# Kernel optimization log

Measured on AMD Instinct MI355X. Metric: run time of the kernel, lower is better.

## Reference

```python
import jax, jax.numpy as jnp
import numpy as np

EPS = 1e-5

def _conv(x, w, b, pad):
    y = jax.lax.conv_general_dilated(x, w, window_strides=(1, 1),
                                     padding=[(pad, pad), (pad, pad)],
                                     dimension_numbers=('NCHW', 'OIHW', 'NCHW'))
    return y + b[None, :, None, None]

def _bn_train(x, gamma, beta):
    # BatchNorm2d in training mode: batch statistics over (N,H,W), biased var
    mean = jnp.mean(x, axis=(0, 2, 3), keepdims=True)
    var = jnp.mean(jnp.square(x - mean), axis=(0, 2, 3), keepdims=True)
    xhat = (x - mean) * jax.lax.rsqrt(var + EPS)
    return xhat * gamma[None, :, None, None] + beta[None, :, None, None]

def _maxpool2(x):
    # CustomMaxPool2d(kernel=2) -> stride=2, no padding applied to data
    return jax.lax.reduce_window(x, -jnp.inf, jax.lax.max,
                                 (1, 1, 2, 2), (1, 1, 2, 2), 'VALID')

def setup_inputs() -> dict:
    key = jax.random.key(0)
    ks = jax.random.split(key, 12)
    B = 64
    d = jax.random.normal(ks[0], (B, 3, 224, 224), dtype=jnp.float32)
    def w_init(k, shape, fan_in):
        bound = 1.0 / np.sqrt(fan_in)
        return jax.random.uniform(k, shape, jnp.float32, -bound, bound)
    conv1_w = w_init(ks[1], (16, 3, 2, 2), 3 * 2 * 2)
    conv1_b = w_init(ks[2], (16,), 3 * 2 * 2)
    conv2_w = w_init(ks[3], (32, 16, 3, 3), 16 * 9)
    conv2_b = w_init(ks[4], (32,), 16 * 9)
    conv3_w = w_init(ks[5], (64, 32, 3, 3), 32 * 9)
    conv3_b = w_init(ks[6], (64,), 32 * 9)
    fc1_w = w_init(ks[7], (256, 64 * 28 * 28), 64 * 28 * 28)
    fc1_b = w_init(ks[8], (256,), 64 * 28 * 28)
    fc2_w = w_init(ks[9], (5, 256), 256)
    fc2_b = w_init(ks[10], (5,), 256)
    return dict(d=d,
                conv1_w=conv1_w, conv1_b=conv1_b,
                bn1_g=jnp.ones((16,), jnp.float32), bn1_b=jnp.zeros((16,), jnp.float32),
                conv2_w=conv2_w, conv2_b=conv2_b,
                bn2_g=jnp.ones((32,), jnp.float32), bn2_b=jnp.zeros((32,), jnp.float32),
                conv3_w=conv3_w, conv3_b=conv3_b,
                bn3_g=jnp.ones((64,), jnp.float32), bn3_b=jnp.zeros((64,), jnp.float32),
                fc1_w=fc1_w, fc1_b=fc1_b, fc2_w=fc2_w, fc2_b=fc2_b)

def reference(d, conv1_w, conv1_b, bn1_g, bn1_b,
              conv2_w, conv2_b, bn2_g, bn2_b,
              conv3_w, conv3_b, bn3_g, bn3_b,
              fc1_w, fc1_b, fc2_w, fc2_b):
    x = _maxpool2(jax.nn.relu(_bn_train(_conv(d, conv1_w, conv1_b, 1), bn1_g, bn1_b)))   # [B,16,112,112]
    x = _maxpool2(jax.nn.relu(_bn_train(_conv(x, conv2_w, conv2_b, 1), bn2_g, bn2_b)))   # [B,32,56,56]
    x = _maxpool2(jax.nn.relu(_bn_train(_conv(x, conv3_w, conv3_b, 1), bn3_g, bn3_b)))   # [B,64,28,28]
    x = x.reshape(x.shape[0], -1)                                                        # [B,50176]
    x = jax.nn.relu(x @ fc1_w.T + fc1_b)
    return x @ fc2_w.T + fc2_b                                                           # [B,5]
```

## Files before the change

### kernel.cpp

```cpp
#include <hip/hip_runtime.h>
#include <cstdint>
#include <cstddef>


typedef __attribute__((ext_vector_type(8))) short sh8_t;
typedef __attribute__((ext_vector_type(4))) float f4_t;
typedef unsigned short u16;
typedef unsigned int u32;

#define WS_X1   ((size_t)0)
#define WS_SEL1 ((size_t)6422528)
#define WS_X2   ((size_t)12845056)
#define WS_SEL2 ((size_t)16056320)
#define WS_X3T  ((size_t)19267584)
#define WS_SEL3 ((size_t)20873216)
#define WS_WT1  ((size_t)22478848)
#define WS_WT2  ((size_t)22479360)
#define WS_WT3  ((size_t)22482432)
#define WS_P1   ((size_t)22491648)
#define WS_P2   ((size_t)24334848)
#define WS_P3   ((size_t)25137664)
#define WS_PD   ((size_t)25596416)
#define WS_ST   ((size_t)25600512)
#define WS_FCP  ((size_t)25600736)
#define WS_H1   ((size_t)26518240)

static __device__ __forceinline__ float4 ldg4(const float* p) {
  return *reinterpret_cast<const float4*>(p);
}
static __device__ __forceinline__ float bf2f(u16 u) {
  union { u32 i; float f; } c; c.i = ((u32)u) << 16; return c.f;
}
static __device__ __forceinline__ u16 f2bf(float f) {
  union { float f; u32 i; } c; c.f = f;
  const u32 x = c.i;
  return (u16)((x + 0x7fffu + ((x >> 16) & 1u)) >> 16);
}

__global__ __launch_bounds__(256)
void k_prep_w(const float* __restrict__ w1, const float* __restrict__ w2,
              const float* __restrict__ w3, u16* __restrict__ wt1,
              u16* __restrict__ wt2, u16* __restrict__ wt3) {
  const int t = blockIdx.x * 256 + threadIdx.x;
  if (t < 1024) {
    const int half = t >> 9;
    const int u = t & 511;
    const int co = u >> 5, k = u & 31;
    const int g = k >> 3, j = k & 7;
    const int kh = g >> 1, kw = g & 1;
    const int ci = (j < 4) ? j : j - 4;
    bool active = (j != 3) && (j != 7);
    if (half == 1) active = active && (j < 4);
    float val = 0.f;
    if (active) {
      const float w = w1[((co * 3 + ci) * 2 + kh) * 2 + kw];
      const u16 h = f2bf(w);
      val = (half == 0) ? bf2f(h) : (w - bf2f(h));
    }
    wt1[t] = f2bf(val);
  } else if (t < 7168) {
    const int u = t - 1024;
    const int ci = u & 15, kwp = (u >> 4) & 3, kh = (u >> 6) % 3, co = u / 192;
    float v = 0.f;
    if (kwp < 3) v = w2[((co * 16 + ci) * 3 + kh) * 3 + kwp];
    wt2[u] = f2bf(v);
  } else {
    const int u = t - 7168;
    const int ci = u & 31, kw = (u >> 5) % 3, kh = (u / 96) % 3, co = u / 288;
    wt3[u] = f2bf(w3[((co * 32 + ci) * 3 + kh) * 3 + kw]);
  }
}

__global__ __launch_bounds__(256)
void k_conv1(const float* __restrict__ d, const u16* __restrict__ wt1,
             const float* __restrict__ b1, const float* __restrict__ g1,
             u16* __restrict__ sel1, float* __restrict__ part) {
  const int bx = blockIdx.x, by = blockIdx.y, n = blockIdx.z;
  const int ow0 = bx * 16, oh0 = by * 16;
  const int t = threadIdx.x, lane = t & 63, wv = t >> 6;
  const int g = lane >> 4, li = lane & 15;
  const int kh = g >> 1, kw = g & 1;
  const sh8_t A1 = *reinterpret_cast<const sh8_t*>(wt1 + li * 32 + g * 8);
  const sh8_t A2 = *reinterpret_cast<const sh8_t*>(wt1 + 512 + li * 32 + g * 8);
  const int iw = ow0 + li + kw - 1;
  const bool iwv = (unsigned)iw < 224u;
  const float* dbase = d + (size_t)n * 3 * 50176 + iw;
  f4_t acc[4];
  #pragma unroll
  for (int r = 0; r < 4; ++r) acc[r] = (f4_t)0.f;
  #pragma unroll
  for (int r = 0; r < 4; ++r) {
    const int ih = oh0 + wv * 4 + r + kh - 1;
    float v0 = 0.f, v1 = 0.f, v2 = 0.f;
    if (iwv && (unsigned)ih < 224u) {
      const float* p = dbase + (size_t)ih * 224;
      v0 = p[0]; v1 = p[50176]; v2 = p[100352];
    }
    const u16 h0 = f2bf(v0), h1 = f2bf(v1), h2 = f2bf(v2);
    const u16 l0 = f2bf(v0 - bf2f(h0));
    const u16 l1 = f2bf(v1 - bf2f(h1));
    const u16 l2 = f2bf(v2 - bf2f(h2));
    union { sh8_t v; u32 w[4]; } B;
    B.w[0] = (u32)h0 | ((u32)h1 << 16);
    B.w[1] = (u32)h2;
    B.w[2] = (u32)l0 | ((u32)l1 << 16);
    B.w[3] = (u32)l2;
    acc[r] = __builtin_amdgcn_mfma_f32_16x16x32_bf16(A1, B.v, acc[r], 0, 0, 0);
    acc[r] = __builtin_amdgcn_mfma_f32_16x16x32_bf16(A2, B.v, acc[r], 0, 0, 0);
  }
  const f4_t bias = *reinterpret_cast<const f4_t*>(b1 + 4 * g);
  const f4_t gam  = *reinterpret_cast<const f4_t*>(g1 + 4 * g);
  f4_t y[4];
  #pragma unroll
  for (int r = 0; r < 4; ++r) y[r] = acc[r] + bias;
  const int ow = ow0 + li;
  {
    f4_t ssum = (f4_t)0.f, ssq = (f4_t)0.f;
    #pragma unroll
    for (int r = 0; r < 4; ++r) {
      const int oh = oh0 + wv * 4 + r;
      if (oh <= 224 && ow <= 224) { ssum += y[r]; ssq += y[r] * y[r]; }
    }
    #pragma unroll
    for (int m = 1; m < 16; m <<= 1)
      #pragma unroll
      for (int j = 0; j < 4; ++j) {
        ssum[j] += __shfl_xor(ssum[j], m);
        ssq[j]  += __shfl_xor(ssq[j], m);
      }
    if (li == 0) {
      const int slot = ((n * 15 + by) * 15 + bx) * 4 + wv;
      #pragma unroll
      for (int j = 0; j < 4; ++j) {
        part[(size_t)((4 * g + j) * 2 + 0) * 57600 + slot] = ssum[j];
        part[(size_t)((4 * g + j) * 2 + 1) * 57600 + slot] = ssq[j];
      }
    }
  }
  if (bx < 14 && by < 14) {
    #pragma unroll
    for (int rp = 0; rp < 2; ++rp) {
      f4_t v;
      #pragma unroll
      for (int j = 0; j < 4; ++j) {
        const float a = y[2 * rp][j], b = y[2 * rp + 1][j];
        v[j] = (gam[j] >= 0.f) ? fmaxf(a, b) : fminf(a, b);
      }
      f4_t o;
      #pragma unroll
      for (int j = 0; j < 4; ++j) o[j] = __shfl_xor(v[j], 1);
      if ((li & 1) == 0) {
        u16 pk[4];
        #pragma unroll
        for (int j = 0; j < 4; ++j)
          pk[j] = f2bf((gam[j] >= 0.f) ? fmaxf(v[j], o[j]) : fminf(v[j], o[j]));
        const int po = 8 * by + 2 * wv + rp, qo = 8 * bx + (li >> 1);
        const size_t off = ((size_t)((n * 112 + po) * 112 + qo)) * 16 + 4 * g;
        uint2 w;
        w.x = (u32)pk[0] | ((u32)pk[1] << 16);
        w.y = (u32)pk[2] | ((u32)pk[3] << 16);
        *reinterpret_cast<uint2*>(sel1 + off) = w;
      }
    }
  }
}

__global__ __launch_bounds__(256)
void k_fin1(const float* __restrict__ part, int P, int chunk, int S,
            double* __restrict__ p2) {
  const int c = blockIdx.x, s = blockIdx.y;
  const int start = s * chunk;
  const int end = min(P, start + chunk);
  __shared__ double rs[256], rq[256];
  double accs[2];
  #pragma unroll
  for (int mom = 0; mom < 2; ++mom) {
    const float* base = part + (size_t)(c * 2 + mom) * P;
    double a0 = 0.0, a1 = 0.0, a2 = 0.0, a3 = 0.0;
    int i = start + threadIdx.x * 4;
    for (; i + 3 < end; i += 1024) {
      const float4 v = ldg4(base + i);
      a0 += v.x; a1 += v.y; a2 += v.z; a3 += v.w;
    }
    for (int j = i; j < end && j < i + 4; ++j) a0 += base[j];
    accs[mom] = (a0 + a1) + (a2 + a3);
  }
  rs[threadIdx.x] = accs[0]; rq[threadIdx.x] = accs[1];
  __syncthreads();
  for (int off = 128; off > 0; off >>= 1) {
    if (threadIdx.x < off) {
      rs[threadIdx.x] += rs[threadIdx.x + off];
      rq[threadIdx.x] += rq[threadIdx.x + off];
    }
    __syncthreads();
  }
  if (threadIdx.x == 0) {
    p2[(size_t)(c * 2 + 0) * S + s] = rs[0];
    p2[(size_t)(c * 2 + 1) * S + s] = rq[0];
  }
}

__global__ __launch_bounds__(64)
void k_fin2(const double* __restrict__ p2, int S, double count,
            const float* __restrict__ g, const float* __restrict__ bta,
            float* __restrict__ scale, float* __restrict__ shift) {
  const int c = blockIdx.x, t = threadIdx.x;
  double s = 0.0, sq = 0.0;
  if (t < S) {
    s  = p2[(size_t)(c * 2 + 0) * S + t];
    sq = p2[(size_t)(c * 2 + 1) * S + t];
  }
  #pragma unroll
  for (int m = 1; m < 64; m <<= 1) {
    s  += __shfl_xor(s, m);
    sq += __shfl_xor(sq, m);
  }
  if (t == 0) {
    const double mean = s / count;
    const double var  = sq / count - mean * mean;
    const double rstd = 1.0 / sqrt(var + 1e-5);
    const double sc = (double)g[c] * rstd;
    scale[c] = (float)sc;
    shift[c] = (float)((double)bta[c] - mean * sc);
  }
}

template<int CH, int P>
__global__ __launch_bounds__(256)
void k_bnrelu(const u16* __restrict__ sel, const float* __restrict__ scale,
              const float* __restrict__ shift, u16* __restrict__ xout) {
  constexpr int G = CH / 8;
  const int idx = blockIdx.x * 256 + threadIdx.x;
  const int cg = idx & (G - 1);
  int rest = idx / G;
  const int qo = rest % P; rest /= P;
  const int po = rest % P;
  const int n = rest / P;
  const size_t base = ((size_t)((n * P + po) * P + qo)) * CH + cg * 8;
  const int4 vs = *reinterpret_cast<const int4*>(sel + base);
  const u32* a = reinterpret_cast<const u32*>(&vs);
  u16 o[8];
  #pragma unroll
  for (int j = 0; j < 8; ++j) {
    const int c = cg * 8 + j;
    const float sc = scale[c], sh = shift[c];
    const u16 raw = (u16)(a[j >> 1] >> ((j & 1) * 16));
    o[j] = f2bf(fmaxf(fmaf(bf2f(raw), sc, sh), 0.f));
  }
  u32 pk[4];
  #pragma unroll
  for (int k = 0; k < 4; ++k) pk[k] = (u32)o[2 * k] | ((u32)o[2 * k + 1] << 16);
  *reinterpret_cast<int4*>(xout + base) = make_int4(pk[0], pk[1], pk[2], pk[3]);
}

__global__ __launch_bounds__(256)
void k_conv2(const u16* __restrict__ x1, const u16* __restrict__ wt2,
             const float* __restrict__ b2, const float* __restrict__ g2,
             u16* __restrict__ sel2, float* __restrict__ part) {
  const int ow0 = blockIdx.x * 16, oh0 = blockIdx.y * 16, n = blockIdx.z;
  const int t = threadIdx.x, lane = t & 63, wv = t >> 6;
  const int g = lane >> 4, li = lane & 15;
  __shared__ __align__(16) unsigned char tile[18 * 640];
  for (int idx = t; idx < 720; idx += 256) {
    const int rr = idx / 40, rem = idx - rr * 40, p = rem >> 1, c = rem & 1;
    const int ih = oh0 - 1 + rr, iw = ow0 - 1 + p;
    int4 v = make_int4(0, 0, 0, 0);
    if ((unsigned)ih < 112u && (unsigned)iw < 112u)
      v = *reinterpret_cast<const int4*>(x1 + ((size_t)((n * 112 + ih) * 112 + iw) * 16 + c * 8));
    *reinterpret_cast<int4*>(tile + ((rr * 640 + p * 32 + c * 16) ^ (((p >> 2) & 1) << 4))) = v;
  }
  sh8_t W[2][3][2];
  #pragma unroll
  for (int cot = 0; cot < 2; ++cot)
    #pragma unroll
    for (int kh = 0; kh < 3; ++kh)
      #pragma unroll
      for (int m = 0; m < 2; ++m)
        W[cot][kh][m] = *reinterpret_cast<const sh8_t*>(
            wt2 + ((cot * 16 + li) * 192 + kh * 64 + m * 32 + g * 8));
  f4_t acc[4][2];
  #pragma unroll
  for (int r = 0; r < 4; ++r) { acc[r][0] = (f4_t)0.f; acc[r][1] = (f4_t)0.f; }
  __syncthreads();
  const int rowb = 4 * wv;
  #pragma unroll
  for (int ihr = 0; ihr < 6; ++ihr) {
    const int row = rowb + ihr;
    #pragma unroll
    for (int m = 0; m < 2; ++m) {
      const int p = li + 2 * m + (g >> 1);
      const sh8_t B = *reinterpret_cast<const sh8_t*>(
          tile + ((row * 640 + p * 32 + (g & 1) * 16) ^ (((p >> 2) & 1) << 4)));
      #pragma unroll
      for (int kh = 0; kh < 3; ++kh) {
        const int r = ihr - kh;
        if (r >= 0 && r < 4) {
          acc[r][0] = __builtin_amdgcn_mfma_f32_16x16x32_bf16(W[0][kh][m], B, acc[r][0], 0, 0, 0);
          acc[r][1] = __builtin_amdgcn_mfma_f32_16x16x32_bf16(W[1][kh][m], B, acc[r][1], 0, 0, 0);
        }
      }
    }
  }
  f4_t bias[2], gam[2], ssum[2], ssq[2];
  bias[0] = *reinterpret_cast<const f4_t*>(b2 + 4 * g);
  bias[1] = *reinterpret_cast<const f4_t*>(b2 + 16 + 4 * g);
  gam[0]  = *reinterpret_cast<const f4_t*>(g2 + 4 * g);
  gam[1]  = *reinterpret_cast<const f4_t*>(g2 + 16 + 4 * g);
  ssum[0] = (f4_t)0.f; ssum[1] = (f4_t)0.f; ssq[0] = (f4_t)0.f; ssq[1] = (f4_t)0.f;
  #pragma unroll
  for (int r = 0; r < 4; ++r)
    #pragma unroll
    for (int cot = 0; cot < 2; ++cot) {
      acc[r][cot] += bias[cot];
      ssum[cot] += acc[r][cot];
      ssq[cot] += acc[r][cot] * acc[r][cot];
    }
  #pragma unroll
  for (int msk = 1; msk < 16; msk <<= 1)
    #pragma unroll
    for (int cot = 0; cot < 2; ++cot)
      #pragma unroll
      for (int j = 0; j < 4; ++j) {
        ssum[cot][j] += __shfl_xor(ssum[cot][j], msk);
        ssq[cot][j]  += __shfl_xor(ssq[cot][j], msk);
      }
  if (li == 0) {
    const int slot = (((n * 7 + (int)blockIdx.y) * 7 + (int)blockIdx.x)) * 4 + wv;
    #pragma unroll
    for (int cot = 0; cot < 2; ++cot)
      #pragma unroll
      for (int j = 0; j < 4; ++j) {
        const int co = cot * 16 + 4 * g + j;
        part[(size_t)(co * 2 + 0) * 12544 + slot] = ssum[cot][j];
        part[(size_t)(co * 2 + 1) * 12544 + slot] = ssq[cot][j];
      }
  }
  const int pob = 8 * (int)blockIdx.y + 2 * wv;
  const int qo = 8 * (int)blockIdx.x + (li >> 1);
  #pragma unroll
  for (int rp = 0; rp < 2; ++rp)
    #pragma unroll
    for (int cot = 0; cot < 2; ++cot) {
      f4_t v;
      #pragma unroll
      for (int j = 0; j < 4; ++j) {
        const float a = acc[2 * rp][cot][j], b = acc[2 * rp + 1][cot][j];
        v[j] = (gam[cot][j] >= 0.f) ? fmaxf(a, b) : fminf(a, b);
      }
      f4_t o;
      #pragma unroll
      for (int j = 0; j < 4; ++j) o[j] = __shfl_xor(v[j], 1);
      if ((li & 1) == 0) {
        u16 pk[4];
        #pragma unroll
        for (int j = 0; j < 4; ++j)
          pk[j] = f2bf((gam[cot][j] >= 0.f) ? fmaxf(v[j], o[j]) : fminf(v[j], o[j]));
        const size_t off = ((size_t)((n * 56 + pob + rp) * 56 + qo)) * 32 + cot * 16 + 4 * g;
        uint2 w;
        w.x = (u32)pk[0] | ((u32)pk[1] << 16);
        w.y = (u32)pk[2] | ((u32)pk[3] << 16);
        *reinterpret_cast<uint2*>(sel2 + off) = w;
      }
    }
}

__global__ __launch_bounds__(256)
void k_conv3(const u16* __restrict__ x2, const u16* __restrict__ wt3,
             const float* __restrict__ b3, const float* __restrict__ g3,
             u16* __restrict__ sel3, float* __restrict__ part) {
  const int ow0 = blockIdx.x * 16, oh0 = blockIdx.y * 8, n = blockIdx.z;
  const int t = threadIdx.x, lane = t & 63, wv = t >> 6;
  const int rh = wv & 1, ch = wv >> 1;
  const int g = lane >> 4, li = lane & 15;
  __shared__ __align__(16) unsigned char tile[10 * 1152];
  for (int idx = t; idx < 720; idx += 256) {
    const int rr = idx / 72, rem = idx - rr * 72, p = rem >> 2, c = rem & 3;
    const int ih = oh0 - 1 + rr, iw = ow0 - 1 + p;
    int4 v = make_int4(0, 0, 0, 0);
    if ((unsigned)ih < 56u && (unsigned)iw < 56u)
      v = *reinterpret_cast<const int4*>(x2 + ((size_t)((n * 56 + ih) * 56 + iw) * 32 + c * 8));
    *reinterpret_cast<int4*>(tile + ((rr * 1152 + p * 64 + c * 16) ^ (((p >> 1) & 3) << 4))) = v;
  }
  sh8_t W[2][3][3];
  #pragma unroll
  for (int c2 = 0; c2 < 2; ++c2)
    #pragma unroll
    for (int kh = 0; kh < 3; ++kh)
      #pragma unroll
      for (int kw = 0; kw < 3; ++kw)
        W[c2][kh][kw] = *reinterpret_cast<const sh8_t*>(
            wt3 + ((size_t)(ch * 32 + c2 * 16 + li) * 288 + (kh * 3 + kw) * 32 + g * 8));
  f4_t acc[4][2];
  #pragma unroll
  for (int r = 0; r < 4; ++r) { acc[r][0] = (f4_t)0.f; acc[r][1] = (f4_t)0.f; }
  __syncthreads();
  const int rowb = 4 * rh;
  #pragma unroll
  for (int ihr = 0; ihr < 6; ++ihr) {
    const int row = rowb + ihr;
    #pragma unroll
    for (int kw = 0; kw < 3; ++kw) {
      const int p = li + kw;
      const sh8_t B = *reinterpret_cast<const sh8_t*>(
          tile + ((row * 1152 + p * 64 + g * 16) ^ (((p >> 1) & 3) << 4)));
      #pragma unroll
      for (int kh = 0; kh < 3; ++kh) {
        const int r = ihr - kh;
        if (r >= 0 && r < 4) {
          acc[r][0] = __builtin_amdgcn_mfma_f32_16x16x32_bf16(W[0][kh][kw], B, acc[r][0], 0, 0, 0);
          acc[r][1] = __builtin_amdgcn_mfma_f32_16x16x32_bf16(W[1][kh][kw], B, acc[r][1], 0, 0, 0);
        }
      }
    }
  }
  const int ow = ow0 + li;
  const bool valid = ow < 56;
  f4_t bias[2], gam[2], ssum[2], ssq[2];
  bias[0] = *reinterpret_cast<const f4_t*>(b3 + ch * 32 + 4 * g);
  bias[1] = *reinterpret_cast<const f4_t*>(b3 + ch * 32 + 16 + 4 * g);
  gam[0]  = *reinterpret_cast<const f4_t*>(g3 + ch * 32 + 4 * g);
  gam[1]  = *reinterpret_cast<const f4_t*>(g3 + ch * 32 + 16 + 4 * g);
  ssum[0] = (f4_t)0.f; ssum[1] = (f4_t)0.f; ssq[0] = (f4_t)0.f; ssq[1] = (f4_t)0.f;
  #pragma unroll
  for (int r = 0; r < 4; ++r)
    #pragma unroll
    for (int c2 = 0; c2 < 2; ++c2) {
      acc[r][c2] += bias[c2];
      if (valid) {
        ssum[c2] += acc[r][c2];
        ssq[c2] += acc[r][c2] * acc[r][c2];
      }
    }
  #pragma unroll
  for (int msk = 1; msk < 16; msk <<= 1)
    #pragma unroll
    for (int c2 = 0; c2 < 2; ++c2)
      #pragma unroll
      for (int j = 0; j < 4; ++j) {
        ssum[c2][j] += __shfl_xor(ssum[c2][j], msk);
        ssq[c2][j]  += __shfl_xor(ssq[c2][j], msk);
      }
  if (li == 0) {
    const int slot = (((n * 7 + (int)blockIdx.y) * 4 + (int)blockIdx.x)) * 2 + rh;
    #pragma unroll
    for (int c2 = 0; c2 < 2; ++c2)
      #pragma unroll
      for (int j = 0; j < 4; ++j) {
        const int co = ch * 32 + c2 * 16 + 4 * g + j;
        part[(size_t)(co * 2 + 0) * 3584 + slot] = ssum[c2][j];
        part[(size_t)(co * 2 + 1) * 3584 + slot] = ssq[c2][j];
      }
  }
  const int pob = 4 * (int)blockIdx.y + 2 * rh;
  const int qo = 8 * (int)blockIdx.x + (li >> 1);
  #pragma unroll
  for (int rp = 0; rp < 2; ++rp)
    #pragma unroll
    for (int c2 = 0; c2 < 2; ++c2) {
      f4_t v;
      #pragma unroll
      for (int j = 0; j < 4; ++j) {
        const float a = acc[2 * rp][c2][j], b = acc[2 * rp + 1][c2][j];
        v[j] = (gam[c2][j] >= 0.f) ? fmaxf(a, b) : fminf(a, b);
      }
      f4_t o;
      #pragma unroll
      for (int j = 0; j < 4; ++j) o[j] = __shfl_xor(v[j], 1);
      if (((li & 1) == 0) && (ow + 1 < 56)) {
        u16 pk[4];
        #pragma unroll
        for (int j = 0; j < 4; ++j)
          pk[j] = f2bf((gam[c2][j] >= 0.f) ? fmaxf(v[j], o[j]) : fminf(v[j], o[j]));
        const size_t off = ((size_t)((n * 28 + pob + rp) * 28 + qo)) * 64 + ch * 32 + c2 * 16 + 4 * g;
        uint2 w;
        w.x = (u32)pk[0] | ((u32)pk[1] << 16);
        w.y = (u32)pk[2] | ((u32)pk[3] << 16);
        *reinterpret_cast<uint2*>(sel3 + off) = w;
      }
    }
}

__global__ __launch_bounds__(256)
void k_bnrelu3t(const u16* __restrict__ sel3, const float* __restrict__ scale,
                const float* __restrict__ shift, u16* __restrict__ x3t) {
  const int n = blockIdx.y;
  const int c = threadIdx.x & 63, pq = threadIdx.x >> 6;
  const int po = blockIdx.x * 4 + pq;
  const float sc = scale[c], sh = shift[c];
  const size_t row0 = ((size_t)(n * 28 + po)) * 28 * 64 + c;
  #pragma unroll
  for (int q4 = 0; q4 < 7; ++q4) {
    u16 pk[4];
    #pragma unroll
    for (int i = 0; i < 4; ++i) {
      const int qo = q4 * 4 + i;
      const u16 raw = sel3[row0 + (size_t)qo * 64];
      pk[i] = f2bf(fmaxf(fmaf(bf2f(raw), sc, sh), 0.f));
    }
    uint2 w;
    w.x = (u32)pk[0] | ((u32)pk[1] << 16);
    w.y = (u32)pk[2] | ((u32)pk[3] << 16);
    *reinterpret_cast<uint2*>(x3t + (((size_t)(n * 64 + c) * 28 + po) * 28 + q4 * 4)) = w;
  }
}

__global__ __launch_bounds__(256)
void k_fc1(const u16* __restrict__ x3t, const float* __restrict__ w,
           float* __restrict__ partial) {
  const int kc = blockIdx.x, nt = blockIdx.y;
  const int t = threadIdx.x, lane = t & 63, wv = t >> 6;
  const int g = lane >> 4, li = lane & 15;
  const int n0 = nt * 64 + wv * 16;
  const float* wrow = w + (size_t)(n0 + li) * 50176 + kc * 896;
  const u16* xbase = x3t + kc * 896;
  f4_t acc[4];
  #pragma unroll
  for (int mf = 0; mf < 4; ++mf) acc[mf] = (f4_t)0.f;
  #pragma unroll 4
  for (int ks = 0; ks < 28; ++ks) {
    const int kb = ks * 32 + g * 8;
    const float4 wa = ldg4(wrow + kb);
    const float4 wb = ldg4(wrow + kb + 4);
    float wf[8] = {wa.x, wa.y, wa.z, wa.w, wb.x, wb.y, wb.z, wb.w};
    sh8_t hi, lo;
    #pragma unroll
    for (int j = 0; j < 8; ++j) {
      const u16 h = f2bf(wf[j]);
      hi[j] = (short)h;
      lo[j] = (short)f2bf(wf[j] - bf2f(h));
    }
    #pragma unroll
    for (int mf = 0; mf < 4; ++mf) {
      const sh8_t B = *reinterpret_cast<const sh8_t*>(
          xbase + (size_t)(mf * 16 + li) * 50176 + kb);
      acc[mf] = __builtin_amdgcn_mfma_f32_16x16x32_bf16(hi, B, acc[mf], 0, 0, 0);
      acc[mf] = __builtin_amdgcn_mfma_f32_16x16x32_bf16(lo, B, acc[mf], 0, 0, 0);
    }
  }
  float* pb = partial + (size_t)kc * 16384;
  #pragma unroll
  for (int mf = 0; mf < 4; ++mf)
    #pragma unroll
    for (int j = 0; j < 4; ++j)
      pb[(size_t)(n0 + 4 * g + j) * 64 + mf * 16 + li] = acc[mf][j];
}

__global__ __launch_bounds__(256)
void k_fc1_reduce(const float* __restrict__ partial, const float* __restrict__ b1f,
                  float* __restrict__ h1) {
  const int idx = blockIdx.x * 256 + threadIdx.x;
  const int nn = idx >> 6, m = idx & 63;
  float a[8];
  #pragma unroll
  for (int u = 0; u < 8; ++u) a[u] = 0.f;
  #pragma unroll
  for (int k = 0; k < 56; k += 8)
    #pragma unroll
    for (int u = 0; u < 8; ++u)
      a[u] += partial[(size_t)(k + u) * 16384 + idx];
  const float s = b1f[nn] + (((a[0] + a[1]) + (a[2] + a[3])) +
                             ((a[4] + a[5]) + (a[6] + a[7])));
  h1[(size_t)m * 256 + nn] = fmaxf(s, 0.f);
}

__global__ __launch_bounds__(320)
void k_fc2(const float* __restrict__ h1, const float* __restrict__ w2f,
           const float* __restrict__ b2f, float* __restrict__ out) {
  const int t = threadIdx.x;
  const int m = t / 5, o = t - m * 5;
  const float* hr = h1 + (size_t)m * 256;
  const float* wr = w2f + (size_t)o * 256;
  float a0 = 0.f, a1 = 0.f, a2 = 0.f, a3 = 0.f;
  #pragma unroll
  for (int j = 0; j < 256; j += 16) {
    const float4 h0 = ldg4(hr + j),      w0 = ldg4(wr + j);
    const float4 h1v = ldg4(hr + j + 4),  w1v = ldg4(wr + j + 4);
    const float4 h2 = ldg4(hr + j + 8),  w2 = ldg4(wr + j + 8);
    const float4 h3 = ldg4(hr + j + 12), w3 = ldg4(wr + j + 12);
    a0 = fmaf(h0.x, w0.x, fmaf(h0.y, w0.y, fmaf(h0.z, w0.z, fmaf(h0.w, w0.w, a0))));
    a1 = fmaf(h1v.x, w1v.x, fmaf(h1v.y, w1v.y, fmaf(h1v.z, w1v.z, fmaf(h1v.w, w1v.w, a1))));
    a2 = fmaf(h2.x, w2.x, fmaf(h2.y, w2.y, fmaf(h2.z, w2.z, fmaf(h2.w, w2.w, a2))));
    a3 = fmaf(h3.x, w3.x, fmaf(h3.y, w3.y, fmaf(h3.z, w3.z, fmaf(h3.w, w3.w, a3))));
  }
  out[m * 5 + o] = b2f[o] + ((a0 + a1) + (a2 + a3));
}

extern "C" void kernel_launch(void* const* d_in, const int* in_sizes, int n_in,
                              void* d_out, int out_size, void* d_ws, size_t ws_size,
                              hipStream_t stream) {
  (void)in_sizes; (void)n_in; (void)out_size; (void)ws_size;
  const float* d   = (const float*)d_in[0];
  const float* w1  = (const float*)d_in[1];
  const float* b1  = (const float*)d_in[2];
  const float* g1  = (const float*)d_in[3];
  const float* be1 = (const float*)d_in[4];
  const float* w2  = (const float*)d_in[5];
  const float* b2  = (const float*)d_in[6];
  const float* g2  = (const float*)d_in[7];
  const float* be2 = (const float*)d_in[8];
  const float* w3  = (const float*)d_in[9];
  const float* b3  = (const float*)d_in[10];
  const float* g3  = (const float*)d_in[11];
  const float* be3 = (const float*)d_in[12];
  const float* fw1 = (const float*)d_in[13];
  const float* fb1 = (const float*)d_in[14];
  const float* fw2 = (const float*)d_in[15];
  const float* fb2 = (const float*)d_in[16];
  float* out = (float*)d_out;
  float* ws  = (float*)d_ws;

  u16* x1   = (u16*)(ws + WS_X1);
  u16* sel1 = (u16*)(ws + WS_SEL1);
  u16* x2   = (u16*)(ws + WS_X2);
  u16* sel2 = (u16*)(ws + WS_SEL2);
  u16* x3t  = (u16*)(ws + WS_X3T);
  u16* sel3 = (u16*)(ws + WS_SEL3);
  u16* wt1  = (u16*)(ws + WS_WT1);
  u16* wt2  = (u16*)(ws + WS_WT2);
  u16* wt3  = (u16*)(ws + WS_WT3);
  float* p1 = ws + WS_P1;
  float* p2 = ws + WS_P2;
  float* p3 = ws + WS_P3;
  double* pd = (double*)(ws + WS_PD);
  float* st = ws + WS_ST;
  float* fcp = ws + WS_FCP;
  float* h1 = ws + WS_H1;

  k_prep_w<<<100, 256, 0, stream>>>(w1, w2, w3, wt1, wt2, wt3);
  k_conv1<<<dim3(15, 15, 64), 256, 0, stream>>>(d, wt1, b1, g1, sel1, p1);
  k_fin1<<<dim3(16, 64), 256, 0, stream>>>(p1, 57600, 900, 64, pd);
  k_fin2<<<16, 64, 0, stream>>>(pd, 64, 3240000.0, g1, be1, st + 0, st + 16);
  k_bnrelu<16, 112><<<6272, 256, 0, stream>>>(sel1, st + 0, st + 16, x1);
  k_conv2<<<dim3(7, 7, 64), 256, 0, stream>>>(x1, wt2, b2, g2, sel2, p2);
  k_fin1<<<dim3(32, 16), 256, 0, stream>>>(p2, 12544, 784, 16, pd);
  k_fin2<<<32, 64, 0, stream>>>(pd, 16, 802816.0, g2, be2, st + 32, st + 64);
  k_bnrelu<32, 56><<<3136, 256, 0, stream>>>(sel2, st + 32, st + 64, x2);
  k_conv3<<<dim3(4, 7, 64), 256, 0, stream>>>(x2, wt3, b3, g3, sel3, p3);
  k_fin1<<<dim3(64, 8), 256, 0, stream>>>(p3, 3584, 448, 8, pd);
  k_fin2<<<64, 64, 0, stream>>>(pd, 8, 200704.0, g3, be3, st + 96, st + 160);
  k_bnrelu3t<<<dim3(7, 64), 256, 0, stream>>>(sel3, st + 96, st + 160, x3t);
  k_fc1<<<dim3(56, 4), 256, 0, stream>>>(x3t, fw1, fcp);
  k_fc1_reduce<<<64, 256, 0, stream>>>(fcp, fb1, h1);
  k_fc2<<<1, 320, 0, stream>>>(h1, fw2, fb2, out);
}
```

Measured before the change: 181.5 us.

## Compute conv1 BN statistics from input autocorrelation moments instead of conv outputs

Result: slower. 214.0 us (+17.9%).

```diff
diff --git a/kernel.cpp b/kernel.cpp
--- a/kernel.cpp
+++ b/kernel.cpp
@@ -8,22 +8,23 @@
 typedef unsigned short u16;
 typedef unsigned int u32;
 
-#define WS_X1   ((size_t)0)
-#define WS_SEL1 ((size_t)6422528)
+#define WS_SEL1 ((size_t)0)
+#define WS_X1   ((size_t)6422528)
 #define WS_X2   ((size_t)12845056)
 #define WS_SEL2 ((size_t)16056320)
+#define WS_REC  WS_X1
 #define WS_X3T  ((size_t)19267584)
 #define WS_SEL3 ((size_t)20873216)
 #define WS_WT1  ((size_t)22478848)
 #define WS_WT2  ((size_t)22479360)
 #define WS_WT3  ((size_t)22482432)
-#define WS_P1   ((size_t)22491648)
-#define WS_P2   ((size_t)24334848)
-#define WS_P3   ((size_t)25137664)
-#define WS_PD   ((size_t)25596416)
-#define WS_ST   ((size_t)25600512)
-#define WS_FCP  ((size_t)25600736)
-#define WS_H1   ((size_t)26518240)
+#define WS_CP   ((size_t)22491648)
+#define WS_P2   ((size_t)23056128)
+#define WS_P3   ((size_t)23858944)
+#define WS_PD   ((size_t)24317696)
+#define WS_ST   ((size_t)24321792)
+#define WS_FCP  ((size_t)24322016)
+#define WS_H1   ((size_t)25239520)
 
 static __device__ __forceinline__ float4 ldg4(const float* p) {
   return *reinterpret_cast<const float4*>(p);
@@ -72,9 +73,157 @@
 }
 
 __global__ __launch_bounds__(256)
-void k_conv1(const float* __restrict__ d, const u16* __restrict__ wt1,
+void k_corr(const float* __restrict__ d, u16* __restrict__ rec,
+            float* __restrict__ cpart) {
+  const int tid = blockIdx.x * 256 + threadIdx.x;
+  const int n = tid / 3136;
+  const int rem = tid - n * 3136;
+  const int ih = rem / 14, seg = rem - ih * 14;
+  const int c0 = seg * 16;
+  float acc[45];
+  #pragma unroll
+  for (int q = 0; q < 45; ++q) acc[q] = 0.f;
+  const bool hasDown = (ih + 1 < 224);
+  #pragma unroll
+  for (int chunk = 0; chunk < 4; ++chunk) {
+    const int c = c0 + chunk * 4;
+    float r0[3][6], r1[3][6];
+    #pragma unroll
+    for (int ci = 0; ci < 3; ++ci) {
+      const float* pr = d + ((size_t)(n * 3 + ci) * 224 + ih) * 224;
+      const float4 v = ldg4(pr + c);
+      r0[ci][1] = v.x; r0[ci][2] = v.y; r0[ci][3] = v.z; r0[ci][4] = v.w;
+      r0[ci][0] = (c > 0) ? pr[c - 1] : 0.f;
+      r0[ci][5] = (c + 4 < 224) ? pr[c + 4] : 0.f;
+      if (hasDown) {
+        const float4 w = ldg4(pr + 224 + c);
+        r1[ci][1] = w.x; r1[ci][2] = w.y; r1[ci][3] = w.z; r1[ci][4] = w.w;
+        r1[ci][0] = (c > 0) ? pr[224 + c - 1] : 0.f;
+        r1[ci][5] = (c + 4 < 224) ? pr[224 + c + 4] : 0.f;
+      } else {
+        #pragma unroll
+        for (int z = 0; z < 6; ++z) r1[ci][z] = 0.f;
+      }
+    }
+    #pragma unroll
+    for (int p = 0; p < 4; ++p) {
+      float a[3];
+      a[0] = r0[0][1 + p]; a[1] = r0[1][1 + p]; a[2] = r0[2][1 + p];
+      acc[42] += a[0]; acc[43] += a[1]; acc[44] += a[2];
+      acc[36] = fmaf(a[0], a[0], acc[36]);
+      acc[37] = fmaf(a[0], a[1], acc[37]);
+      acc[38] = fmaf(a[0], a[2], acc[38]);
+      acc[39] = fmaf(a[1], a[1], acc[39]);
+      acc[40] = fmaf(a[1], a[2], acc[40]);
+      acc[41] = fmaf(a[2], a[2], acc[41]);
+      #pragma unroll
+      for (int i = 0; i < 3; ++i)
+        #pragma unroll
+        for (int j = 0; j < 3; ++j)
+          acc[27 + i * 3 + j] = fmaf(a[i], r0[j][2 + p], acc[27 + i * 3 + j]);
+      #pragma unroll
+      for (int i = 0; i < 3; ++i)
+        #pragma unroll
+        for (int j = 0; j < 3; ++j)
+          #pragma unroll
+          for (int dwp = 0; dwp < 3; ++dwp)
+            acc[(i * 3 + j) * 3 + dwp] =
+                fmaf(a[i], r1[j][p + dwp], acc[(i * 3 + j) * 3 + dwp]);
+    }
+    #pragma unroll
+    for (int p = 0; p < 4; ++p) {
+      const float v0 = r0[0][1 + p], v1 = r0[1][1 + p], v2 = r0[2][1 + p];
+      const u16 h0 = f2bf(v0), h1 = f2bf(v1), h2 = f2bf(v2);
+      int4 rr;
+      rr.x = (u32)h0 | ((u32)h1 << 16);
+      rr.y = (u32)h2;
+      rr.z = (u32)f2bf(v0 - bf2f(h0)) | ((u32)f2bf(v1 - bf2f(h1)) << 16);
+      rr.w = (u32)f2bf(v2 - bf2f(h2));
+      *reinterpret_cast<int4*>(rec + (size_t)((n * 224 + ih) * 224 + c + p) * 8) = rr;
+    }
+  }
+  #pragma unroll
+  for (int m = 1; m < 16; m <<= 1)
+    #pragma unroll
+    for (int q = 0; q < 45; ++q) acc[q] += __shfl_xor(acc[q], m);
+  if ((threadIdx.x & 15) == 0) {
+    const int slot = blockIdx.x * 16 + (threadIdx.x >> 4);
+    #pragma unroll
+    for (int q = 0; q < 45; ++q) cpart[q * 12544 + slot] = acc[q];
+  }
+}
+
+__global__ __launch_bounds__(256)
+void k_corr_fin(const float* __restrict__ cpart, double* __restrict__ pd45) {
+  const int q = blockIdx.x;
+  const float* base = cpart + q * 12544;
+  double a0 = 0, a1 = 0, a2 = 0, a3 = 0;
+  for (int i = threadIdx.x * 4; i + 3 < 12544; i += 1024) {
+    const float4 v = ldg4(base + i);
+    a0 += v.x; a1 += v.y; a2 += v.z; a3 += v.w;
+  }
+  __shared__ double rs[256];
+  rs[threadIdx.x] = (a0 + a1) + (a2 + a3);
+  __syncthreads();
+  for (int off = 128; off > 0; off >>= 1) {
+    if (threadIdx.x < off) rs[threadIdx.x] += rs[threadIdx.x + off];
+    __syncthreads();
+  }
+  if (threadIdx.x == 0) pd45[q] = rs[0];
+}
+
+__global__ __launch_bounds__(64)
+void k_stats1(const double* __restrict__ pd45, const float* __restrict__ w1,
+              const float* __restrict__ b1, const float* __restrict__ g1,
+              const float* __restrict__ be1, float* __restrict__ scale,
+              float* __restrict__ shift) {
+  const int co = threadIdx.x;
+  if (co >= 16) return;
+  double w[3][2][2];
+  for (int ci = 0; ci < 3; ++ci)
+    for (int kh = 0; kh < 2; ++kh)
+      for (int kw = 0; kw < 2; ++kw)
+        w[ci][kh][kw] = (double)w1[((co * 3 + ci) * 2 + kh) * 2 + kw];
+  double sum_s = 0.0;
+  for (int ci = 0; ci < 3; ++ci)
+    for (int kh = 0; kh < 2; ++kh)
+      for (int kw = 0; kw < 2; ++kw)
+        sum_s += w[ci][kh][kw] * pd45[42 + ci];
+  double ss = 0.0;
+  for (int i = 0; i < 3; ++i)
+    for (int kh = 0; kh < 2; ++kh)
+      for (int kw = 0; kw < 2; ++kw)
+        for (int j = 0; j < 3; ++j)
+          for (int kh2 = 0; kh2 < 2; ++kh2)
+            for (int kw2 = 0; kw2 < 2; ++kw2) {
+              int a = i, b2 = j, dh = kh2 - kh, dw = kw2 - kw;
+              if (dh < 0 || (dh == 0 && dw < 0)) {
+                const int tt = a; a = b2; b2 = tt; dh = -dh; dw = -dw;
+              }
+              double cv;
+              if (dh == 1) cv = pd45[(a * 3 + b2) * 3 + dw + 1];
+              else if (dw == 1) cv = pd45[27 + a * 3 + b2];
+              else {
+                const int lo = (a < b2) ? a : b2, hi = (a < b2) ? b2 : a;
+                cv = pd45[36 + lo * (5 - lo) / 2 + hi];
+              }
+              ss += w[i][kh][kw] * w[j][kh2][kw2] * cv;
+            }
+  const double Npos = 3240000.0;
+  const double b = (double)b1[co];
+  const double mu = sum_s / Npos + b;
+  const double E2 = (ss + 2.0 * b * sum_s) / Npos + b * b;
+  const double var = E2 - mu * mu;
+  const double rstd = 1.0 / sqrt(var + 1e-5);
+  const double sc = (double)g1[co] * rstd;
+  scale[co] = (float)sc;
+  shift[co] = (float)((double)be1[co] - mu * sc);
+}
+
+__global__ __launch_bounds__(256)
+void k_conv1(const u16* __restrict__ rec, const u16* __restrict__ wt1,
              const float* __restrict__ b1, const float* __restrict__ g1,
-             u16* __restrict__ sel1, float* __restrict__ part) {
+             u16* __restrict__ sel1) {
   const int bx = blockIdx.x, by = blockIdx.y, n = blockIdx.z;
   const int ow0 = bx * 16, oh0 = by * 16;
   const int t = threadIdx.x, lane = t & 63, wv = t >> 6;
@@ -83,84 +232,45 @@
   const sh8_t A1 = *reinterpret_cast<const sh8_t*>(wt1 + li * 32 + g * 8);
   const sh8_t A2 = *reinterpret_cast<const sh8_t*>(wt1 + 512 + li * 32 + g * 8);
   const int iw = ow0 + li + kw - 1;
-  const bool iwv = (unsigned)iw < 224u;
-  const float* dbase = d + (size_t)n * 3 * 50176 + iw;
+  const bool iwv = iw >= 0;
   f4_t acc[4];
   #pragma unroll
   for (int r = 0; r < 4; ++r) acc[r] = (f4_t)0.f;
   #pragma unroll
   for (int r = 0; r < 4; ++r) {
     const int ih = oh0 + wv * 4 + r + kh - 1;
-    float v0 = 0.f, v1 = 0.f, v2 = 0.f;
-    if (iwv && (unsigned)ih < 224u) {
-      const float* p = dbase + (size_t)ih * 224;
-      v0 = p[0]; v1 = p[50176]; v2 = p[100352];
-    }
-    const u16 h0 = f2bf(v0), h1 = f2bf(v1), h2 = f2bf(v2);
-    const u16 l0 = f2bf(v0 - bf2f(h0));
-    const u16 l1 = f2bf(v1 - bf2f(h1));
-    const u16 l2 = f2bf(v2 - bf2f(h2));
-    union { sh8_t v; u32 w[4]; } B;
-    B.w[0] = (u32)h0 | ((u32)h1 << 16);
-    B.w[1] = (u32)h2;
-    B.w[2] = (u32)l0 | ((u32)l1 << 16);
-    B.w[3] = (u32)l2;
-    acc[r] = __builtin_amdgcn_mfma_f32_16x16x32_bf16(A1, B.v, acc[r], 0, 0, 0);
-    acc[r] = __builtin_amdgcn_mfma_f32_16x16x32_bf16(A2, B.v, acc[r], 0, 0, 0);
+    sh8_t B = (sh8_t)(short)0;
+    if (iwv && ih >= 0)
+      B = *reinterpret_cast<const sh8_t*>(rec + (size_t)((n * 224 + ih) * 224 + iw) * 8);
+    acc[r] = __builtin_amdgcn_mfma_f32_16x16x32_bf16(A1, B, acc[r], 0, 0, 0);
+    acc[r] = __builtin_amdgcn_mfma_f32_16x16x32_bf16(A2, B, acc[r], 0, 0, 0);
   }
   const f4_t bias = *reinterpret_cast<const f4_t*>(b1 + 4 * g);
   const f4_t gam  = *reinterpret_cast<const f4_t*>(g1 + 4 * g);
   f4_t y[4];
   #pragma unroll
   for (int r = 0; r < 4; ++r) y[r] = acc[r] + bias;
-  const int ow = ow0 + li;
-  {
-    f4_t ssum = (f4_t)0.f, ssq = (f4_t)0.f;
-    #pragma unroll
-    for (int r = 0; r < 4; ++r) {
-      const int oh = oh0 + wv * 4 + r;
-      if (oh <= 224 && ow <= 224) { ssum += y[r]; ssq += y[r] * y[r]; }
-    }
-    #pragma unroll
-    for (int m = 1; m < 16; m <<= 1)
-      #pragma unroll
-      for (int j = 0; j < 4; ++j) {
-        ssum[j] += __shfl_xor(ssum[j], m);
-        ssq[j]  += __shfl_xor(ssq[j], m);
-      }
-    if (li == 0) {
-      const int slot = ((n * 15 + by) * 15 + bx) * 4 + wv;
-      #pragma unroll
-      for (int j = 0; j < 4; ++j) {
-        part[(size_t)((4 * g + j) * 2 + 0) * 57600 + slot] = ssum[j];
-        part[(size_t)((4 * g + j) * 2 + 1) * 57600 + slot] = ssq[j];
-      }
-    }
-  }
-  if (bx < 14 && by < 14) {
-    #pragma unroll
-    for (int rp = 0; rp < 2; ++rp) {
-      f4_t v;
-      #pragma unroll
-      for (int j = 0; j < 4; ++j) {
-        const float a = y[2 * rp][j], b = y[2 * rp + 1][j];
-        v[j] = (gam[j] >= 0.f) ? fmaxf(a, b) : fminf(a, b);
-      }
-      f4_t o;
-      #pragma unroll
-      for (int j = 0; j < 4; ++j) o[j] = __shfl_xor(v[j], 1);
-      if ((li & 1) == 0) {
-        u16 pk[4];
-        #pragma unroll
-        for (int j = 0; j < 4; ++j)
-          pk[j] = f2bf((gam[j] >= 0.f) ? fmaxf(v[j], o[j]) : fminf(v[j], o[j]));
-        const int po = 8 * by + 2 * wv + rp, qo = 8 * bx + (li >> 1);
-        const size_t off = ((size_t)((n * 112 + po) * 112 + qo)) * 16 + 4 * g;
-        uint2 w;
-        w.x = (u32)pk[0] | ((u32)pk[1] << 16);
-        w.y = (u32)pk[2] | ((u32)pk[3] << 16);
-        *reinterpret_cast<uint2*>(sel1 + off) = w;
-      }
+  #pragma unroll
+  for (int rp = 0; rp < 2; ++rp) {
+    f4_t v;
+    #pragma unroll
+    for (int j = 0; j < 4; ++j) {
+      const float a = y[2 * rp][j], b = y[2 * rp + 1][j];
+      v[j] = (gam[j] >= 0.f) ? fmaxf(a, b) : fminf(a, b);
+    }
+    f4_t o;
+    #pragma unroll
+    for (int j = 0; j < 4; ++j) o[j] = __shfl_xor(v[j], 1);
+    if ((li & 1) == 0) {
+      u16 pk[4];
+      #pragma unroll
+      for (int j = 0; j < 4; ++j)
+        pk[j] = f2bf((gam[j] >= 0.f) ? fmaxf(v[j], o[j]) : fminf(v[j], o[j]));
+      const int po = 8 * by + 2 * wv + rp, qo = 8 * bx + (li >> 1);
+      uint2 w;
+      w.x = (u32)pk[0] | ((u32)pk[1] << 16);
+      w.y = (u32)pk[2] | ((u32)pk[3] << 16);
+      *reinterpret_cast<uint2*>(sel1 + ((size_t)((n * 112 + po) * 112 + qo)) * 16 + 4 * g) = w;
     }
   }
 }
@@ -609,8 +719,9 @@
   float* out = (float*)d_out;
   float* ws  = (float*)d_ws;
 
+  u16* sel1 = (u16*)(ws + WS_SEL1);
   u16* x1   = (u16*)(ws + WS_X1);
-  u16* sel1 = (u16*)(ws + WS_SEL1);
+  u16* rec  = (u16*)(ws + WS_REC);
   u16* x2   = (u16*)(ws + WS_X2);
   u16* sel2 = (u16*)(ws + WS_SEL2);
   u16* x3t  = (u16*)(ws + WS_X3T);
@@ -618,7 +729,7 @@
   u16* wt1  = (u16*)(ws + WS_WT1);
   u16* wt2  = (u16*)(ws + WS_WT2);
   u16* wt3  = (u16*)(ws + WS_WT3);
-  float* p1 = ws + WS_P1;
+  float* cp = ws + WS_CP;
   float* p2 = ws + WS_P2;
   float* p3 = ws + WS_P3;
   double* pd = (double*)(ws + WS_PD);
@@ -627,9 +738,10 @@
   float* h1 = ws + WS_H1;
 
   k_prep_w<<<100, 256, 0, stream>>>(w1, w2, w3, wt1, wt2, wt3);
-  k_conv1<<<dim3(15, 15, 64), 256, 0, stream>>>(d, wt1, b1, g1, sel1, p1);
-  k_fin1<<<dim3(16, 64), 256, 0, stream>>>(p1, 57600, 900, 64, pd);
-  k_fin2<<<16, 64, 0, stream>>>(pd, 64, 3240000.0, g1, be1, st + 0, st + 16);
+  k_corr<<<784, 256, 0, stream>>>(d, rec, cp);
+  k_corr_fin<<<45, 256, 0, stream>>>(cp, pd);
+  k_stats1<<<1, 64, 0, stream>>>(pd, w1, b1, g1, be1, st + 0, st + 16);
+  k_conv1<<<dim3(14, 14, 64), 256, 0, stream>>>(rec, wt1, b1, g1, sel1);
   k_bnrelu<16, 112><<<6272, 256, 0, stream>>>(sel1, st + 0, st + 16, x1);
   k_conv2<<<dim3(7, 7, 64), 256, 0, stream>>>(x1, wt2, b2, g2, sel2, p2);
   k_fin1<<<dim3(32, 16), 256, 0, stream>>>(p2, 12544, 784, 16, pd);
```
